# Kernel tuning notes

Measured on AMD Instinct MI355X. Metric: run time of the kernel, lower is better.

The kernel has to match this reference:

```python
import jax, jax.numpy as jnp
import numpy as np
import math

B, T, D, H = 2, 2048, 2048, 16
HD = D // H  # head_dim = 128


def setup_inputs() -> dict:
    key = jax.random.key(0)
    ks = jax.random.split(key, 9)
    s = 1.0 / math.sqrt(D)
    return {
        "x": jax.random.normal(ks[0], (B, T, D), dtype=jnp.float32),
        "Wq": jax.random.normal(ks[1], (D, D), dtype=jnp.float32) * s,
        "bq": jax.random.normal(ks[2], (D,), dtype=jnp.float32) * 0.01,
        "Wk": jax.random.normal(ks[3], (D, D), dtype=jnp.float32) * s,
        "bk": jax.random.normal(ks[4], (D,), dtype=jnp.float32) * 0.01,
        "Wv": jax.random.normal(ks[5], (D, D), dtype=jnp.float32) * s,
        "bv": jax.random.normal(ks[6], (D,), dtype=jnp.float32) * 0.01,
        "Wo": jax.random.normal(ks[7], (D, D), dtype=jnp.float32) * s,
        "bo": jax.random.normal(ks[8], (D,), dtype=jnp.float32) * 0.01,
    }


def reference(x, Wq, bq, Wk, bk, Wv, bv, Wo, bo):
    b, t, c = x.shape
    # projections; split heads: (B,T,D) -> (B,H,T,HD)
    def split_heads(y):
        return y.reshape(b, t, H, HD).transpose(0, 2, 1, 3)

    q = split_heads(x @ Wq + bq)
    k = split_heads(x @ Wk + bk)
    v = split_heads(x @ Wv + bv)

    scale = 1.0 / math.sqrt(HD)
    attn = jnp.einsum('bhqd,bhkd->bhqk', q, k) * scale  # (B,H,T,T)
    # causal mask (prefill path: past_k is None)
    causal = jnp.tril(jnp.ones((t, t), dtype=bool))
    attn = jnp.where(causal, attn, -jnp.inf)
    attn = jax.nn.softmax(attn, axis=-1)
    out = jnp.einsum('bhqk,bhkd->bhqd', attn, v)  # (B,H,T,HD)
    out = out.transpose(0, 2, 1, 3).reshape(b, t, c)
    out = out @ Wo + bo
    return (out, k, v)
```

## Files before the change

kernel.cpp:

```cpp
#include <hip/hip_runtime.h>
#include <hip/hip_bf16.h>

#define B_ 2
#define T_ 2048
#define D_ 2048
#define H_ 16
#define HD_ 128
#define M_ 4096

typedef __attribute__((ext_vector_type(8))) short short8;
typedef __attribute__((ext_vector_type(8))) __bf16 bf16x8;
typedef __attribute__((ext_vector_type(4))) float f32x4;
typedef __attribute__((ext_vector_type(4))) unsigned uint32x4;

__device__ __forceinline__ short f2bf(float f) {
  unsigned u = __builtin_bit_cast(unsigned, f);
  u += 0x7fffu + ((u >> 16) & 1u);
  return (short)(u >> 16);
}

__device__ __forceinline__ unsigned pk2(float lo, float hi) {
  return ((unsigned)(unsigned short)f2bf(hi) << 16) |
         (unsigned)(unsigned short)f2bf(lo);
}

__device__ __forceinline__ void gl_lds16(const void* g, void* l) {
  __builtin_amdgcn_global_load_lds(
      (const __attribute__((address_space(1))) unsigned int*)g,
      (__attribute__((address_space(3))) unsigned int*)l, 16, 0, 0);
}

__device__ __forceinline__ f32x4 mfma_bf16(short8 a, short8 b, f32x4 c) {
  return __builtin_amdgcn_mfma_f32_16x16x32_bf16(
      __builtin_bit_cast(bf16x8, a), __builtin_bit_cast(bf16x8, b), c, 0, 0, 0);
}

__device__ __forceinline__ float2 sw16f(float x) {
  float a = x, bv;
  asm("v_mov_b32 %0, %1" : "=v"(bv) : "v"(x));
  asm("v_permlane16_swap_b32 %0, %1" : "+v"(a), "+v"(bv));
  return make_float2(a, bv);
}
__device__ __forceinline__ float2 sw32f(float x) {
  float a = x, bv;
  asm("v_mov_b32 %0, %1" : "=v"(bv) : "v"(x));
  asm("v_permlane32_swap_b32 %0, %1" : "+v"(a), "+v"(bv));
  return make_float2(a, bv);
}
__device__ __forceinline__ void sw16u(unsigned x, unsigned& e, unsigned& o) {
  unsigned a = x, bv;
  asm("v_mov_b32 %0, %1" : "=v"(bv) : "v"(x));
  asm("v_permlane16_swap_b32 %0, %1" : "+v"(a), "+v"(bv));
  e = a; o = bv;
}
__device__ __forceinline__ void pl32u(unsigned& a, unsigned& b) {
  asm("v_permlane32_swap_b32 %0, %1" : "+v"(a), "+v"(b));
}

__global__ void cast_f32_bf16(const float* __restrict__ in, short* __restrict__ out, int n4) {
  int i = blockIdx.x * blockDim.x + threadIdx.x;
  int stride = gridDim.x * blockDim.x;
  for (; i < n4; i += stride) {
    float4 v = ((const float4*)in)[i];
    short4 s;
    s.x = f2bf(v.x); s.y = f2bf(v.y); s.z = f2bf(v.z); s.w = f2bf(v.w);
    ((short4*)out)[i] = s;
  }
}

__global__ void transpose_cast_w4(const float* __restrict__ Wq, const float* __restrict__ Wk,
                                  const float* __restrict__ Wv, const float* __restrict__ Wo,
                                  short* __restrict__ wqkv, short* __restrict__ wo) {
  __shared__ float t[32][33];
  int z = blockIdx.z;
  const float* W = z == 0 ? Wq : z == 1 ? Wk : z == 2 ? Wv : Wo;
  short* dst = z < 3 ? wqkv + (size_t)z * D_ * D_ : wo;
  int n0 = blockIdx.x * 32, k0 = blockIdx.y * 32;
  int tx = threadIdx.x, ty = threadIdx.y;
#pragma unroll
  for (int j = 0; j < 4; ++j)
    t[ty + j * 8][tx] = W[(size_t)(k0 + ty + j * 8) * D_ + n0 + tx];
  __syncthreads();
#pragma unroll
  for (int j = 0; j < 4; ++j)
    dst[(size_t)(n0 + ty + j * 8) * D_ + k0 + tx] = f2bf(t[tx][ty + j * 8]);
}

__global__ void transpose_v(const short* __restrict__ vb, short* __restrict__ vtb) {
  __shared__ short t[32][33];
  int bh = blockIdx.z;
  int t0 = blockIdx.x * 32, h0 = blockIdx.y * 32;
  int tx = threadIdx.x, ty = threadIdx.y;
  const short* src = vb + (size_t)bh * T_ * HD_;
  short* dst = vtb + (size_t)bh * HD_ * T_;
#pragma unroll
  for (int j = 0; j < 4; ++j)
    t[ty + j * 8][tx] = src[(size_t)(t0 + ty + j * 8) * HD_ + h0 + tx];
  __syncthreads();
#pragma unroll
  for (int j = 0; j < 4; ++j)
    dst[(size_t)(h0 + ty + j * 8) * T_ + t0 + tx] = t[tx][ty + j * 8];
}

template <int MODE>
__global__ __launch_bounds__(256, 2) void gemm_rb(
    const short* __restrict__ A, const short* __restrict__ Bt,
    const float* __restrict__ b0, const float* __restrict__ b1,
    const float* __restrict__ b2,
    short* __restrict__ q_o, short* __restrict__ k_o, short* __restrict__ v_o,
    float* __restrict__ kf_o, float* __restrict__ vf_o, float* __restrict__ f_o) {
  __shared__ __attribute__((aligned(16))) short lds[4][2][4096];
  const int K = D_, NT = K / 32;

  int nx = gridDim.x, nwg = nx * gridDim.y;
  int d = blockIdx.y * nx + blockIdx.x;
  int cpx = nwg >> 3;
  int lg = (d & 7) * cpx + (d >> 3);
  int m0 = (lg / nx) * 128, n0 = (lg % nx) * 128;

  int tid = threadIdx.x, lane = tid & 63, w = tid >> 6;
  int wm = w >> 1, wn = w & 1;
  int lr = lane & 15, g = lane >> 4;

  int o1 = tid * 16, o2 = 4096 + tid * 16;
  int row1 = tid >> 2, row2 = 64 + row1;
  int cb = (tid & 3) << 4;
  int c1 = (cb ^ (((row1 >> 1) & 3) << 4)) >> 1;
  int c2 = (cb ^ (((row2 >> 1) & 3) << 4)) >> 1;
  const short* aS1 = A + (size_t)(m0 + row1) * K + c1;
  const short* aS2 = A + (size_t)(m0 + row2) * K + c2;
  const short* bS1 = Bt + (size_t)(n0 + row1) * K + c1;
  const short* bS2 = Bt + (size_t)(n0 + row2) * K + c2;

  int aoff[4], boff[4];
#pragma unroll
  for (int i = 0; i < 4; ++i) {
    int ra = wm * 64 + i * 16 + lr;
    aoff[i] = ra * 64 + ((g * 16) ^ (((ra >> 1) & 3) << 4));
    int rb = wn * 64 + i * 16 + lr;
    boff[i] = rb * 64 + ((g * 16) ^ (((rb >> 1) & 3) << 4));
  }

  f32x4 acc[4][4] = {};

#pragma unroll
  for (int s = 0; s < 3; ++s) {
    char* la = (char*)&lds[s][0][0];
    char* lb = (char*)&lds[s][1][0];
    gl_lds16(aS1 + s * 32, la + o1);
    gl_lds16(aS2 + s * 32, la + o2);
    gl_lds16(bS1 + s * 32, lb + o1);
    gl_lds16(bS2 + s * 32, lb + o2);
  }
  asm volatile("s_waitcnt vmcnt(8)" ::: "memory");
  __builtin_amdgcn_s_barrier();
  __builtin_amdgcn_sched_barrier(0);

#pragma unroll 1
  for (int t4 = 0; t4 < NT; t4 += 4) {
#pragma unroll
    for (int p = 0; p < 4; ++p) {
      int t = t4 + p;
      {
        int ts = (t + 3 < NT) ? t + 3 : NT - 1;
        char* la = (char*)&lds[(p + 3) & 3][0][0];
        char* lb = (char*)&lds[(p + 3) & 3][1][0];
        gl_lds16(aS1 + ts * 32, la + o1);
        gl_lds16(aS2 + ts * 32, la + o2);
        gl_lds16(bS1 + ts * 32, lb + o1);
        gl_lds16(bS2 + ts * 32, lb + o2);
      }
      const char* la = (const char*)&lds[p][0][0];
      const char* lb = (const char*)&lds[p][1][0];
      short8 af[4], bfv[4];
#pragma unroll
      for (int i = 0; i < 4; ++i) {
        af[i] = *(const short8*)(la + aoff[i]);
        bfv[i] = *(const short8*)(lb + boff[i]);
      }
      __builtin_amdgcn_s_setprio(1);
#pragma unroll
      for (int mi = 0; mi < 4; ++mi)
#pragma unroll
        for (int ni = 0; ni < 4; ++ni)
          acc[mi][ni] = mfma_bf16(af[mi], bfv[ni], acc[mi][ni]);
      __builtin_amdgcn_s_setprio(0);
      asm volatile("s_waitcnt vmcnt(8)" ::: "memory");
      __builtin_amdgcn_s_barrier();
      __builtin_amdgcn_sched_barrier(0);
    }
  }

  if (MODE == 0) {
    int region = n0 >> 11;
    int nc = n0 & 2047;
    const float* bias = region == 0 ? b0 : region == 1 ? b1 : b2;
    short* obf = region == 0 ? q_o : region == 1 ? k_o : v_o;
    float* of32 = region == 1 ? kf_o : region == 2 ? vf_o : nullptr;
#pragma unroll
    for (int mi = 0; mi < 4; ++mi) {
#pragma unroll
      for (int ni = 0; ni < 4; ++ni) {
        int gr0 = m0 + wm * 64 + mi * 16 + (g << 2);
        int gc = nc + wn * 64 + ni * 16 + lr;
        float bv = bias[gc];
#pragma unroll
        for (int r = 0; r < 4; ++r) {
          int gr = gr0 + r;
          float v = acc[mi][ni][r] + bv;
          int bb = gr >> 11, tt = gr & (T_ - 1), hh = gc >> 7, hd = gc & (HD_ - 1);
          size_t idx = (((size_t)(bb * H_ + hh) * T_) + tt) * HD_ + hd;
          obf[idx] = f2bf(v);
          if (of32) of32[idx] = v;
        }
      }
    }
  } else {
#pragma unroll
    for (int mi = 0; mi < 4; ++mi) {
#pragma unroll
      for (int ni = 0; ni < 4; ++ni) {
        int gr0 = m0 + wm * 64 + mi * 16 + (g << 2);
        int gc = n0 + wn * 64 + ni * 16 + lr;
        float bv = b0[gc];
#pragma unroll
        for (int r = 0; r < 4; ++r)
          f_o[(size_t)(gr0 + r) * D_ + gc] = acc[mi][ni][r] + bv;
      }
    }
  }
}

__global__ __launch_bounds__(256, 2) void attn_fwd(
    const short* __restrict__ qb, const short* __restrict__ kb,
    const short* __restrict__ vtb, short* __restrict__ aob) {
  __shared__ __attribute__((aligned(16))) char kvlds[2][16384];

  int d = blockIdx.y * gridDim.x + blockIdx.x;
  int lg = (d & 7) * 64 + (d >> 3);
  int bh = lg >> 4, jx = lg & 15;

  int tid = threadIdx.x, w = tid >> 6, lane = tid & 63;
  int lr = lane & 15, g = lane >> 4;
  const short* Q  = qb  + (size_t)bh * T_ * HD_;
  const short* Kp = kb  + (size_t)bh * T_ * HD_;
  const short* Vt = vtb + (size_t)bh * HD_ * T_;
  const float scale = 0.08838834764831845f;
  int b = bh >> 4, h = bh & 15;
  bool hi16 = (lane & 16) != 0;

  int oA = ((2 * w + 0) * 64 + lane) * 16;
  int oB = ((2 * w + 1) * 64 + lane) * 16;
  int rKA = oA >> 8, rKB = oB >> 8;
  size_t skA = (size_t)rKA * HD_ + (((oA & 255) ^ ((rKA & 7) << 4)) >> 1);
  size_t skB = (size_t)rKB * HD_ + (((oB & 255) ^ ((rKB & 7) << 4)) >> 1);
  int rVA = oA >> 6, rVB = oB >> 6;
  size_t svA = (size_t)rVA * T_ + (((oA & 63) ^ (((rVA >> 1) & 3) << 4)) >> 1);
  size_t svB = (size_t)rVB * T_ + (((oB & 63) ^ (((rVB >> 1) & 3) << 4)) >> 1);

#pragma unroll 1
  for (int pass = 0; pass < 2; ++pass) {
    int qt = pass ? (31 - jx) : jx;
    int q0 = qt * 64 + w * 16;
    int ntiles = 2 * qt + 2;

    {
      char* kd = &kvlds[0][0];
      char* vd = &kvlds[0][8192];
      gl_lds16(Kp + skA, kd + oA);
      gl_lds16(Kp + skB, kd + oB);
      gl_lds16(Vt + svA, vd + oA);
      gl_lds16(Vt + svB, vd + oB);
    }

    short8 qf[4];
#pragma unroll
    for (int kk = 0; kk < 4; ++kk)
      qf[kk] = *(const short8*)&Q[(size_t)(q0 + lr) * HD_ + kk * 32 + g * 8];

    f32x4 o[8] = {};
    float mrow = -1e30f, lrow = 0.f;
    __syncthreads();

#pragma unroll 1
    for (int t = 0; t < ntiles; ++t) {
      int kv0 = t * 32, buf = t & 1;
      if (t + 1 < ntiles) {
        char* kd = &kvlds[buf ^ 1][0];
        char* vd = &kvlds[buf ^ 1][8192];
        const short* Kn = Kp + (size_t)(kv0 + 32) * HD_;
        const short* Vn = Vt + (kv0 + 32);
        gl_lds16(Kn + skA, kd + oA);
        gl_lds16(Kn + skB, kd + oB);
        gl_lds16(Vn + svA, vd + oA);
        gl_lds16(Vn + svB, vd + oB);
      }
      if (kv0 < q0 + 16) {
        const char* kb_ = &kvlds[buf][0];
        const char* vb_ = &kvlds[buf][8192];
        short8 kf0[4], kf1[4], vf[8];
#pragma unroll
        for (int kk = 0; kk < 4; ++kk) {
          int cs = (kk * 64 + g * 16) ^ ((lr & 7) << 4);
          kf0[kk] = *(const short8*)(kb_ + (lr * 256 + cs));
          kf1[kk] = *(const short8*)(kb_ + ((16 + lr) * 256 + cs));
        }
#pragma unroll
        for (int f = 0; f < 8; ++f)
          vf[f] = *(const short8*)(vb_ + ((f * 16 + lr) * 64 +
                   ((g * 16) ^ (((lr >> 1) & 3) << 4))));

        f32x4 s0 = {}, s1 = {};
        __builtin_amdgcn_s_setprio(1);
#pragma unroll
        for (int kk = 0; kk < 4; ++kk) {
          s0 = mfma_bf16(kf0[kk], qf[kk], s0);
          s1 = mfma_bf16(kf1[kk], qf[kk], s1);
        }
        __builtin_amdgcn_s_setprio(0);

        float vv[8];
#pragma unroll
        for (int r = 0; r < 4; ++r) {
          vv[r] = s0[r] * scale;
          vv[4 + r] = s1[r] * scale;
        }
        if (kv0 + 31 > q0) {
          int qrow = q0 + lr;
#pragma unroll
          for (int r = 0; r < 4; ++r) {
            if (kv0 + 4 * g + r > qrow) vv[r] = -1e30f;
            if (kv0 + 16 + 4 * g + r > qrow) vv[4 + r] = -1e30f;
          }
        }

        float pm = vv[0];
#pragma unroll
        for (int i = 1; i < 8; ++i) pm = fmaxf(pm, vv[i]);
        { float2 tpm = sw32f(pm); pm = fmaxf(tpm.x, tpm.y); }
        { float2 tpm = sw16f(pm); pm = fmaxf(tpm.x, tpm.y); }

        bool rescale = !__all(pm - mrow <= 8.0f);
        float alpha = 1.0f;
        if (rescale) {
          float mnew = fmaxf(mrow, pm);
          alpha = __expf(mrow - mnew);
          mrow = mnew;
        }

        float p[8];
        float rs = 0.f;
#pragma unroll
        for (int i = 0; i < 8; ++i) { p[i] = __expf(vv[i] - mrow); rs += p[i]; }
        { float2 trs = sw32f(rs); rs = trs.x + trs.y; }
        { float2 trs = sw16f(rs); rs = trs.x + trs.y; }
        lrow = (rescale ? lrow * alpha : lrow) + rs;

        if (rescale) {
          float alr[4];
#pragma unroll
          for (int r = 0; r < 4; ++r) alr[r] = __shfl(alpha, 4 * g + r);
#pragma unroll
          for (int f = 0; f < 8; ++f)
#pragma unroll
            for (int r = 0; r < 4; ++r) o[f][r] *= alr[r];
        }

        unsigned w0 = pk2(p[0], p[1]), w1 = pk2(p[2], p[3]);
        unsigned w2 = pk2(p[4], p[5]), w3 = pk2(p[6], p[7]);
        unsigned e0, od0, e1, od1, e2, od2, e3, od3;
        sw16u(w0, e0, od0); sw16u(w1, e1, od1);
        sw16u(w2, e2, od2); sw16u(w3, e3, od3);
        unsigned F0 = e0,  S0 = e2;  pl32u(F0, S0);
        unsigned F1 = e1,  S1 = e3;  pl32u(F1, S1);
        unsigned F2 = od0, S2 = od2; pl32u(F2, S2);
        unsigned F3 = od1, S3 = od3; pl32u(F3, S3);
        uint32x4 paw = { hi16 ? S0 : F0, hi16 ? S1 : F1,
                         hi16 ? S2 : F2, hi16 ? S3 : F3 };
        short8 pa = __builtin_bit_cast(short8, paw);

        __builtin_amdgcn_s_setprio(1);
#pragma unroll
        for (int f = 0; f < 8; ++f) o[f] = mfma_bf16(pa, vf[f], o[f]);
        __builtin_amdgcn_s_setprio(0);
      }
      __syncthreads();
    }

    float inv = 1.0f / lrow;
    float invr[4];
#pragma unroll
    for (int r = 0; r < 4; ++r) invr[r] = __shfl(inv, 4 * g + r);
#pragma unroll
    for (int r = 0; r < 4; ++r) {
      int q = q0 + 4 * g + r;
      size_t rowoff = ((size_t)(b * T_ + q)) * D_ + h * HD_;
#pragma unroll
      for (int f = 0; f < 8; ++f)
        aob[rowoff + f * 16 + lr] = f2bf(o[f][r] * invr[r]);
    }
  }
}

extern "C" void kernel_launch(void* const* d_in, const int* in_sizes, int n_in,
                              void* d_out, int out_size, void* d_ws, size_t ws_size,
                              hipStream_t stream) {
  const float* x  = (const float*)d_in[0];
  const float* Wq = (const float*)d_in[1];
  const float* bq = (const float*)d_in[2];
  const float* Wk = (const float*)d_in[3];
  const float* bk = (const float*)d_in[4];
  const float* Wv = (const float*)d_in[5];
  const float* bv = (const float*)d_in[6];
  const float* Wo = (const float*)d_in[7];
  const float* bo = (const float*)d_in[8];
  float* out  = (float*)d_out;
  float* kout = out + (size_t)M_ * D_;
  float* vout = kout + (size_t)M_ * D_;

  char* ws = (char*)d_ws;
  auto alloc = [&](size_t bytes) {
    char* p = ws;
    ws += (bytes + 255) & ~(size_t)255;
    return p;
  };
  short* xb    = (short*)alloc((size_t)M_ * D_ * 2);
  short* wqkvT = (short*)alloc((size_t)3 * D_ * D_ * 2);
  short* woT   = (short*)alloc((size_t)D_ * D_ * 2);
  short* qb    = (short*)alloc((size_t)M_ * D_ * 2);
  short* kb    = (short*)alloc((size_t)M_ * D_ * 2);
  short* vb    = (short*)alloc((size_t)M_ * D_ * 2);
  short* vtb = wqkvT;
  short* aob = xb;

  cast_f32_bf16<<<2048, 256, 0, stream>>>(x, xb, M_ * D_ / 4);
  dim3 tb(32, 8);
  transpose_cast_w4<<<dim3(64, 64, 4), tb, 0, stream>>>(Wq, Wk, Wv, Wo, wqkvT, woT);

  gemm_rb<0><<<dim3(48, 32), 256, 0, stream>>>(
      xb, wqkvT, bq, bk, bv, qb, kb, vb, kout, vout, nullptr);
  transpose_v<<<dim3(T_ / 32, HD_ / 32, B_ * H_), tb, 0, stream>>>(vb, vtb);
  attn_fwd<<<dim3(16, 32), 256, 0, stream>>>(qb, kb, vtb, aob);
  gemm_rb<1><<<dim3(16, 32), 256, 0, stream>>>(
      aob, woT, bo, nullptr, nullptr, nullptr, nullptr, nullptr,
      nullptr, nullptr, out);
}
```

Baseline: 293.4 us.

## Use 256x256-tile 8-wave GEMM with split-phase LDS pipeline for QKV projection

Replaces the QKV projection GEMM (128x128 tiles, 256 threads) with a dedicated kernel using 256x256 output tiles, 512 threads and a BK=64 double-buffered LDS pipeline. Global-to-LDS loads are interleaved across four MFMA sub-phases. The larger tile raises arithmetic intensity and cuts global and LDS traffic per FLOP for the largest GEMM. In exchange it uses more LDS and registers (128 KB LDS, 32 accumulators per wave) and launches only 384 workgroups, which may hurt occupancy and wave balance.

```diff
diff --git a/kernel.cpp b/kernel.cpp
--- a/kernel.cpp
+++ b/kernel.cpp
@@ -102,13 +102,142 @@
     dst[(size_t)(h0 + ty + j * 8) * T_ + t0 + tx] = t[tx][ty + j * 8];
 }
 
-template <int MODE>
-__global__ __launch_bounds__(256, 2) void gemm_rb(
+__global__ __launch_bounds__(512, 2) void gemm_qkv(
     const short* __restrict__ A, const short* __restrict__ Bt,
     const float* __restrict__ b0, const float* __restrict__ b1,
     const float* __restrict__ b2,
     short* __restrict__ q_o, short* __restrict__ k_o, short* __restrict__ v_o,
-    float* __restrict__ kf_o, float* __restrict__ vf_o, float* __restrict__ f_o) {
+    float* __restrict__ kf_o, float* __restrict__ vf_o) {
+  __shared__ __attribute__((aligned(16))) short lds[2][2][2][8192];
+  const int K = D_, NT = K / 64, NX = 24;
+
+  int d = blockIdx.x;
+  int lg = (d & 7) * 48 + (d >> 3);
+  int m0 = (lg / NX) * 256, n0 = (lg % NX) * 256;
+
+  int tid = threadIdx.x, lane = tid & 63, wid = tid >> 6;
+  int wm = wid >> 2, wn = wid & 3;
+  int lr = lane & 15, g = lane >> 4;
+
+  int sr = tid >> 2;
+  int sc = (((tid & 3) << 4) ^ ((sr & 3) << 4)) >> 1;
+  const short* aSrc = A + (size_t)(m0 + sr) * K + sc;
+  const short* bSrc = Bt + (size_t)(n0 + sr) * K + sc;
+  char* ldsb = (char*)lds;
+
+  auto stage = [&](int ts, int kh, int mat) {
+    char* dst = ldsb + ((((ts & 1) * 2 + kh) * 2 + mat) << 14) + tid * 16;
+    const short* s = (mat == 0 ? aSrc : bSrc) + ts * 64 + kh * 32;
+    gl_lds16(s, dst);
+    gl_lds16(s + (size_t)128 * K, dst + 8192);
+  };
+
+  int swz = (g * 16) ^ ((lr & 3) << 4);
+  int aoffl = (wm * 128 + lr) * 64 + swz;
+  int boffl = (wn * 64 + lr) * 64 + swz;
+
+  f32x4 acc[8][4] = {};
+
+  stage(0, 0, 0); stage(0, 0, 1); stage(0, 1, 0); stage(0, 1, 1);
+  stage(1, 0, 0); stage(1, 0, 1); stage(1, 1, 0);
+  asm volatile("s_waitcnt vmcnt(10)" ::: "memory");
+  __builtin_amdgcn_s_barrier();
+  __builtin_amdgcn_sched_barrier(0);
+
+#pragma unroll 1
+  for (int t = 0; t < NT; ++t) {
+    const char* La = ldsb + (t & 1) * 65536 + aoffl;
+    const char* Lb = ldsb + (t & 1) * 65536 + 16384 + boffl;
+    int t1 = (t + 1 < NT) ? t + 1 : NT - 1;
+    int t2 = (t + 2 < NT) ? t + 2 : NT - 1;
+    short8 afr[8], bf0, bf1;
+
+#pragma unroll
+    for (int mi = 0; mi < 8; ++mi) afr[mi] = *(const short8*)(La + mi * 1024);
+    bf0 = *(const short8*)(Lb);
+    bf1 = *(const short8*)(Lb + 1024);
+    stage(t1, 1, 1);
+    __builtin_amdgcn_s_setprio(1);
+#pragma unroll
+    for (int mi = 0; mi < 8; ++mi) {
+      acc[mi][0] = mfma_bf16(afr[mi], bf0, acc[mi][0]);
+      acc[mi][1] = mfma_bf16(afr[mi], bf1, acc[mi][1]);
+    }
+    __builtin_amdgcn_s_setprio(0);
+    __builtin_amdgcn_s_barrier();
+    __builtin_amdgcn_sched_barrier(0);
+
+    bf0 = *(const short8*)(Lb + 2048);
+    bf1 = *(const short8*)(Lb + 3072);
+    stage(t2, 0, 0);
+    asm volatile("s_waitcnt vmcnt(10)" ::: "memory");
+    __builtin_amdgcn_s_setprio(1);
+#pragma unroll
+    for (int mi = 0; mi < 8; ++mi) {
+      acc[mi][2] = mfma_bf16(afr[mi], bf0, acc[mi][2]);
+      acc[mi][3] = mfma_bf16(afr[mi], bf1, acc[mi][3]);
+    }
+    __builtin_amdgcn_s_setprio(0);
+    __builtin_amdgcn_s_barrier();
+    __builtin_amdgcn_sched_barrier(0);
+
+#pragma unroll
+    for (int mi = 0; mi < 8; ++mi) afr[mi] = *(const short8*)(La + 32768 + mi * 1024);
+    bf0 = *(const short8*)(Lb + 32768);
+    bf1 = *(const short8*)(Lb + 32768 + 1024);
+    stage(t2, 0, 1);
+    __builtin_amdgcn_s_setprio(1);
+#pragma unroll
+    for (int mi = 0; mi < 8; ++mi) {
+      acc[mi][0] = mfma_bf16(afr[mi], bf0, acc[mi][0]);
+      acc[mi][1] = mfma_bf16(afr[mi], bf1, acc[mi][1]);
+    }
+    __builtin_amdgcn_s_setprio(0);
+    __builtin_amdgcn_s_barrier();
+    __builtin_amdgcn_sched_barrier(0);
+
+    bf0 = *(const short8*)(Lb + 32768 + 2048);
+    bf1 = *(const short8*)(Lb + 32768 + 3072);
+    stage(t2, 1, 0);
+    asm volatile("s_waitcnt vmcnt(10)" ::: "memory");
+    __builtin_amdgcn_s_setprio(1);
+#pragma unroll
+    for (int mi = 0; mi < 8; ++mi) {
+      acc[mi][2] = mfma_bf16(afr[mi], bf0, acc[mi][2]);
+      acc[mi][3] = mfma_bf16(afr[mi], bf1, acc[mi][3]);
+    }
+    __builtin_amdgcn_s_setprio(0);
+    __builtin_amdgcn_s_barrier();
+    __builtin_amdgcn_sched_barrier(0);
+  }
+
+  int region = n0 >> 11, nc = n0 & 2047;
+  const float* bias = region == 0 ? b0 : region == 1 ? b1 : b2;
+  short* obf = region == 0 ? q_o : region == 1 ? k_o : v_o;
+  float* of32 = region == 1 ? kf_o : region == 2 ? vf_o : nullptr;
+#pragma unroll
+  for (int mi = 0; mi < 8; ++mi) {
+#pragma unroll
+    for (int ni = 0; ni < 4; ++ni) {
+      int gr0 = m0 + wm * 128 + mi * 16 + (g << 2);
+      int gc = nc + wn * 64 + ni * 16 + lr;
+      float bv = bias[gc];
+#pragma unroll
+      for (int r = 0; r < 4; ++r) {
+        int gr = gr0 + r;
+        float v = acc[mi][ni][r] + bv;
+        int bb = gr >> 11, tt = gr & (T_ - 1), hh = gc >> 7, hd = gc & (HD_ - 1);
+        size_t idx = (((size_t)(bb * H_ + hh) * T_) + tt) * HD_ + hd;
+        obf[idx] = f2bf(v);
+        if (of32) of32[idx] = v;
+      }
+    }
+  }
+}
+
+__global__ __launch_bounds__(256, 2) void gemm_rb(
+    const short* __restrict__ A, const short* __restrict__ Bt,
+    const float* __restrict__ b0, float* __restrict__ f_o) {
   __shared__ __attribute__((aligned(16))) short lds[4][2][4096];
   const int K = D_, NT = K / 32;
 
@@ -191,42 +320,16 @@
     }
   }
 
-  if (MODE == 0) {
-    int region = n0 >> 11;
-    int nc = n0 & 2047;
-    const float* bias = region == 0 ? b0 : region == 1 ? b1 : b2;
-    short* obf = region == 0 ? q_o : region == 1 ? k_o : v_o;
-    float* of32 = region == 1 ? kf_o : region == 2 ? vf_o : nullptr;
-#pragma unroll
-    for (int mi = 0; mi < 4; ++mi) {
-#pragma unroll
-      for (int ni = 0; ni < 4; ++ni) {
-        int gr0 = m0 + wm * 64 + mi * 16 + (g << 2);
-        int gc = nc + wn * 64 + ni * 16 + lr;
-        float bv = bias[gc];
-#pragma unroll
-        for (int r = 0; r < 4; ++r) {
-          int gr = gr0 + r;
-          float v = acc[mi][ni][r] + bv;
-          int bb = gr >> 11, tt = gr & (T_ - 1), hh = gc >> 7, hd = gc & (HD_ - 1);
-          size_t idx = (((size_t)(bb * H_ + hh) * T_) + tt) * HD_ + hd;
-          obf[idx] = f2bf(v);
-          if (of32) of32[idx] = v;
-        }
-      }
-    }
-  } else {
-#pragma unroll
-    for (int mi = 0; mi < 4; ++mi) {
-#pragma unroll
-      for (int ni = 0; ni < 4; ++ni) {
-        int gr0 = m0 + wm * 64 + mi * 16 + (g << 2);
-        int gc = n0 + wn * 64 + ni * 16 + lr;
-        float bv = b0[gc];
-#pragma unroll
-        for (int r = 0; r < 4; ++r)
-          f_o[(size_t)(gr0 + r) * D_ + gc] = acc[mi][ni][r] + bv;
-      }
+#pragma unroll
+  for (int mi = 0; mi < 4; ++mi) {
+#pragma unroll
+    for (int ni = 0; ni < 4; ++ni) {
+      int gr0 = m0 + wm * 64 + mi * 16 + (g << 2);
+      int gc = n0 + wn * 64 + ni * 16 + lr;
+      float bv = b0[gc];
+#pragma unroll
+      for (int r = 0; r < 4; ++r)
+        f_o[(size_t)(gr0 + r) * D_ + gc] = acc[mi][ni][r] + bv;
     }
   }
 }
@@ -437,11 +540,8 @@
   dim3 tb(32, 8);
   transpose_cast_w4<<<dim3(64, 64, 4), tb, 0, stream>>>(Wq, Wk, Wv, Wo, wqkvT, woT);
 
-  gemm_rb<0><<<dim3(48, 32), 256, 0, stream>>>(
-      xb, wqkvT, bq, bk, bv, qb, kb, vb, kout, vout, nullptr);
+  gemm_qkv<<<384, 512, 0, stream>>>(xb, wqkvT, bq, bk, bv, qb, kb, vb, kout, vout);
   transpose_v<<<dim3(T_ / 32, HD_ / 32, B_ * H_), tb, 0, stream>>>(vb, vtb);
   attn_fwd<<<dim3(16, 32), 256, 0, stream>>>(qb, kb, vtb, aob);
-  gemm_rb<1><<<dim3(16, 32), 256, 0, stream>>>(
-      aob, woT, bo, nullptr, nullptr, nullptr, nullptr, nullptr,
-      nullptr, nullptr, out);
-}
+  gemm_rb<<<dim3(16, 32), 256, 0, stream>>>(aob, woT, bo, out);
+}
```

Measured after the change: 275.3 us. 6.2% less time.

## Add dedicated 256x192-tile QKV GEMM that writes transposed V directly

Applied to the files above, without the earlier changes.

Replaces the templated QKV GEMM with a new 512-thread kernel using 256x192 tiles, a 64-wide K step, double-buffered LDS and a 512-workgroup grid sized to the machine. Its epilogue writes bf16 V already transposed per head, so the separate transpose_v kernel and its extra round trip through memory are removed. V-transpose now gets its own workspace buffer instead of reusing the weight buffer. The large LDS footprint and the 8x3 accumulator array may limit occupancy, and the transposed stores are narrow strided writes.

```diff
diff --git a/kernel.cpp b/kernel.cpp
--- a/kernel.cpp
+++ b/kernel.cpp
@@ -86,29 +86,138 @@
     dst[(size_t)(n0 + ty + j * 8) * D_ + k0 + tx] = f2bf(t[tx][ty + j * 8]);
 }
 
-__global__ void transpose_v(const short* __restrict__ vb, short* __restrict__ vtb) {
-  __shared__ short t[32][33];
-  int bh = blockIdx.z;
-  int t0 = blockIdx.x * 32, h0 = blockIdx.y * 32;
-  int tx = threadIdx.x, ty = threadIdx.y;
-  const short* src = vb + (size_t)bh * T_ * HD_;
-  short* dst = vtb + (size_t)bh * HD_ * T_;
-#pragma unroll
-  for (int j = 0; j < 4; ++j)
-    t[ty + j * 8][tx] = src[(size_t)(t0 + ty + j * 8) * HD_ + h0 + tx];
-  __syncthreads();
-#pragma unroll
-  for (int j = 0; j < 4; ++j)
-    dst[(size_t)(h0 + ty + j * 8) * T_ + t0 + tx] = t[tx][ty + j * 8];
-}
-
-template <int MODE>
-__global__ __launch_bounds__(256, 2) void gemm_rb(
+__global__ __launch_bounds__(512, 2) void gemm_qkv(
     const short* __restrict__ A, const short* __restrict__ Bt,
     const float* __restrict__ b0, const float* __restrict__ b1,
     const float* __restrict__ b2,
-    short* __restrict__ q_o, short* __restrict__ k_o, short* __restrict__ v_o,
-    float* __restrict__ kf_o, float* __restrict__ vf_o, float* __restrict__ f_o) {
+    short* __restrict__ q_o, short* __restrict__ k_o,
+    float* __restrict__ kf_o, float* __restrict__ vf_o,
+    short* __restrict__ vt_o) {
+  __shared__ __attribute__((aligned(16))) char lds[2][57344];
+  const int K = D_, NT = K / 64;
+
+  int d = blockIdx.x;
+  int lg = (d & 7) * 64 + (d >> 3);
+  int m0 = (lg & 15) * 256, n0 = (lg >> 4) * 192;
+
+  int tid = threadIdx.x, lane = tid & 63, wid = tid >> 6;
+  int wm = wid >> 2, wn = wid & 3;
+  int lr = lane & 15, g = lane >> 4;
+
+  int rowA = tid >> 2;
+  int cA = ((((tid & 3) << 4) ^ (((rowA >> 1) & 3) << 4)) >> 1);
+  const short* aS = A + (size_t)(m0 + rowA) * K + cA;
+  int rowB = tid >> 3;
+  int cB = ((((tid & 7) << 4) ^ ((rowB & 7) << 4)) >> 1);
+  const short* bS = Bt + (size_t)(n0 + rowB) * K + cB;
+  char* ldsb = (char*)lds;
+
+  auto stageA = [&](int ts, int kh) {
+    char* dst = ldsb + (ts & 1) * 57344 + kh * 16384 + tid * 16;
+    const short* s = aS + ts * 64 + kh * 32;
+    gl_lds16(s, dst);
+    gl_lds16(s + (size_t)128 * K, dst + 8192);
+  };
+  auto stageB = [&](int ts) {
+    char* dst = ldsb + (ts & 1) * 57344 + 32768 + tid * 16;
+    const short* s = bS + ts * 64;
+    gl_lds16(s, dst);
+    gl_lds16(s + (size_t)64 * K, dst + 8192);
+    gl_lds16(s + (size_t)128 * K, dst + 16384);
+  };
+
+  int swzA = (g * 16) ^ (((lr >> 1) & 3) << 4);
+  int aoff = (wm * 128 + lr) * 64 + swzA;
+  int boff0 = (wn * 48 + lr) * 128 + ((g * 16) ^ ((lr & 7) << 4));
+  int boff1 = (wn * 48 + lr) * 128 + (((64 + g * 16)) ^ ((lr & 7) << 4));
+
+  f32x4 acc[8][3] = {};
+
+  stageA(0, 0); stageB(0); stageA(0, 1); stageA(1, 0);
+  asm volatile("s_waitcnt vmcnt(4)" ::: "memory");
+  __builtin_amdgcn_s_barrier();
+  __builtin_amdgcn_sched_barrier(0);
+
+#pragma unroll 1
+  for (int t = 0; t < NT; ++t) {
+    const char* base = ldsb + (t & 1) * 57344;
+    int t1 = (t + 1 < NT) ? t + 1 : NT - 1;
+    int t2 = (t + 2 < NT) ? t + 2 : NT - 1;
+    short8 afr[8], bfr[3];
+
+#pragma unroll
+    for (int mi = 0; mi < 8; ++mi) afr[mi] = *(const short8*)(base + aoff + mi * 1024);
+#pragma unroll
+    for (int ni = 0; ni < 3; ++ni) bfr[ni] = *(const short8*)(base + 32768 + boff0 + ni * 2048);
+    stageA(t1, 1); stageB(t1);
+    __builtin_amdgcn_s_setprio(1);
+#pragma unroll
+    for (int mi = 0; mi < 8; ++mi)
+#pragma unroll
+      for (int ni = 0; ni < 3; ++ni)
+        acc[mi][ni] = mfma_bf16(afr[mi], bfr[ni], acc[mi][ni]);
+    __builtin_amdgcn_s_setprio(0);
+    asm volatile("s_waitcnt vmcnt(7)" ::: "memory");
+    __builtin_amdgcn_s_barrier();
+    __builtin_amdgcn_sched_barrier(0);
+
+#pragma unroll
+    for (int mi = 0; mi < 8; ++mi) afr[mi] = *(const short8*)(base + 16384 + aoff + mi * 1024);
+#pragma unroll
+    for (int ni = 0; ni < 3; ++ni) bfr[ni] = *(const short8*)(base + 32768 + boff1 + ni * 2048);
+    stageA(t2, 0);
+    __builtin_amdgcn_s_setprio(1);
+#pragma unroll
+    for (int mi = 0; mi < 8; ++mi)
+#pragma unroll
+      for (int ni = 0; ni < 3; ++ni)
+        acc[mi][ni] = mfma_bf16(afr[mi], bfr[ni], acc[mi][ni]);
+    __builtin_amdgcn_s_setprio(0);
+    asm volatile("s_waitcnt vmcnt(2)" ::: "memory");
+    __builtin_amdgcn_s_barrier();
+    __builtin_amdgcn_sched_barrier(0);
+  }
+
+#pragma unroll
+  for (int ni = 0; ni < 3; ++ni) {
+    int gcb = n0 + wn * 48 + ni * 16;
+    int region = gcb >> 11;
+    int nc = (gcb & 2047) + lr;
+    int hh = nc >> 7, hd = nc & 127;
+    const float* bias = region == 0 ? b0 : region == 1 ? b1 : b2;
+    float bv = bias[nc];
+#pragma unroll
+    for (int mi = 0; mi < 8; ++mi) {
+      int gr0 = m0 + wm * 128 + mi * 16 + (g << 2);
+      int bb = gr0 >> 11, tt0 = gr0 & 2047;
+      size_t hbase = (size_t)(bb * H_ + hh);
+      float v0 = acc[mi][ni][0] + bv;
+      float v1 = acc[mi][ni][1] + bv;
+      float v2 = acc[mi][ni][2] + bv;
+      float v3 = acc[mi][ni][3] + bv;
+      size_t ib = (hbase * T_ + tt0) * HD_ + hd;
+      if (region == 0) {
+        q_o[ib] = f2bf(v0); q_o[ib + HD_] = f2bf(v1);
+        q_o[ib + 2 * HD_] = f2bf(v2); q_o[ib + 3 * HD_] = f2bf(v3);
+      } else if (region == 1) {
+        k_o[ib] = f2bf(v0); k_o[ib + HD_] = f2bf(v1);
+        k_o[ib + 2 * HD_] = f2bf(v2); k_o[ib + 3 * HD_] = f2bf(v3);
+        kf_o[ib] = v0; kf_o[ib + HD_] = v1;
+        kf_o[ib + 2 * HD_] = v2; kf_o[ib + 3 * HD_] = v3;
+      } else {
+        vf_o[ib] = v0; vf_o[ib + HD_] = v1;
+        vf_o[ib + 2 * HD_] = v2; vf_o[ib + 3 * HD_] = v3;
+        short4 s4;
+        s4.x = f2bf(v0); s4.y = f2bf(v1); s4.z = f2bf(v2); s4.w = f2bf(v3);
+        *(short4*)&vt_o[(hbase * HD_ + hd) * T_ + tt0] = s4;
+      }
+    }
+  }
+}
+
+__global__ __launch_bounds__(256, 2) void gemm_rb(
+    const short* __restrict__ A, const short* __restrict__ Bt,
+    const float* __restrict__ b0, float* __restrict__ f_o) {
   __shared__ __attribute__((aligned(16))) short lds[4][2][4096];
   const int K = D_, NT = K / 32;
 
@@ -191,42 +300,16 @@
     }
   }
 
-  if (MODE == 0) {
-    int region = n0 >> 11;
-    int nc = n0 & 2047;
-    const float* bias = region == 0 ? b0 : region == 1 ? b1 : b2;
-    short* obf = region == 0 ? q_o : region == 1 ? k_o : v_o;
-    float* of32 = region == 1 ? kf_o : region == 2 ? vf_o : nullptr;
-#pragma unroll
-    for (int mi = 0; mi < 4; ++mi) {
-#pragma unroll
-      for (int ni = 0; ni < 4; ++ni) {
-        int gr0 = m0 + wm * 64 + mi * 16 + (g << 2);
-        int gc = nc + wn * 64 + ni * 16 + lr;
-        float bv = bias[gc];
-#pragma unroll
-        for (int r = 0; r < 4; ++r) {
-          int gr = gr0 + r;
-          float v = acc[mi][ni][r] + bv;
-          int bb = gr >> 11, tt = gr & (T_ - 1), hh = gc >> 7, hd = gc & (HD_ - 1);
-          size_t idx = (((size_t)(bb * H_ + hh) * T_) + tt) * HD_ + hd;
-          obf[idx] = f2bf(v);
-          if (of32) of32[idx] = v;
-        }
-      }
-    }
-  } else {
-#pragma unroll
-    for (int mi = 0; mi < 4; ++mi) {
-#pragma unroll
-      for (int ni = 0; ni < 4; ++ni) {
-        int gr0 = m0 + wm * 64 + mi * 16 + (g << 2);
-        int gc = n0 + wn * 64 + ni * 16 + lr;
-        float bv = b0[gc];
-#pragma unroll
-        for (int r = 0; r < 4; ++r)
-          f_o[(size_t)(gr0 + r) * D_ + gc] = acc[mi][ni][r] + bv;
-      }
+#pragma unroll
+  for (int mi = 0; mi < 4; ++mi) {
+#pragma unroll
+    for (int ni = 0; ni < 4; ++ni) {
+      int gr0 = m0 + wm * 64 + mi * 16 + (g << 2);
+      int gc = n0 + wn * 64 + ni * 16 + lr;
+      float bv = b0[gc];
+#pragma unroll
+      for (int r = 0; r < 4; ++r)
+        f_o[(size_t)(gr0 + r) * D_ + gc] = acc[mi][ni][r] + bv;
     }
   }
 }
@@ -429,19 +512,14 @@
   short* woT   = (short*)alloc((size_t)D_ * D_ * 2);
   short* qb    = (short*)alloc((size_t)M_ * D_ * 2);
   short* kb    = (short*)alloc((size_t)M_ * D_ * 2);
-  short* vb    = (short*)alloc((size_t)M_ * D_ * 2);
-  short* vtb = wqkvT;
+  short* vtb   = (short*)alloc((size_t)M_ * D_ * 2);
   short* aob = xb;
 
   cast_f32_bf16<<<2048, 256, 0, stream>>>(x, xb, M_ * D_ / 4);
   dim3 tb(32, 8);
   transpose_cast_w4<<<dim3(64, 64, 4), tb, 0, stream>>>(Wq, Wk, Wv, Wo, wqkvT, woT);
 
-  gemm_rb<0><<<dim3(48, 32), 256, 0, stream>>>(
-      xb, wqkvT, bq, bk, bv, qb, kb, vb, kout, vout, nullptr);
-  transpose_v<<<dim3(T_ / 32, HD_ / 32, B_ * H_), tb, 0, stream>>>(vb, vtb);
+  gemm_qkv<<<512, 512, 0, stream>>>(xb, wqkvT, bq, bk, bv, qb, kb, kout, vout, vtb);
   attn_fwd<<<dim3(16, 32), 256, 0, stream>>>(qb, kb, vtb, aob);
-  gemm_rb<1><<<dim3(16, 32), 256, 0, stream>>>(
-      aob, woT, bo, nullptr, nullptr, nullptr, nullptr, nullptr,
-      nullptr, nullptr, out);
-}
+  gemm_rb<<<dim3(16, 32), 256, 0, stream>>>(aob, woT, bo, out);
+}
```

Measured after the change: 256.4 us. 12.6% less time.
